# Kernel tuning notes

Measured on AMD Instinct MI355X. Metric: run time of the kernel, lower is better.

Reference implementation:

```python
import jax, jax.numpy as jnp
import numpy as np

DIM = 1024
HEADS = 16
DHEAD = 64
MAXLEN = 512
B = 8
N = 256   # sequence (x) length
M = 256   # memory (h) length; M + N <= MAXLEN
INNER = HEADS * DHEAD


def setup_inputs() -> dict:
    key = jax.random.key(0)
    ks = jax.random.split(key, 8)
    w = lambda k, shape: jax.random.normal(k, shape, jnp.float32) * 0.02
    return {
        "x": jax.random.normal(ks[0], (B, N, DIM), jnp.float32),
        "h": jax.random.normal(ks[1], (B, M, DIM), jnp.float32),
        "Wqkv": w(ks[2], (DIM, 3 * INNER)),
        "Wkr": w(ks[3], (DIM, INNER)),
        "R": jax.random.normal(ks[4], (2 * MAXLEN, DIM), jnp.float32),
        "u": jax.random.normal(ks[5], (DHEAD,), jnp.float32),
        "v": jax.random.normal(ks[6], (DHEAD,), jnp.float32),
        "Wout": w(ks[7], (INNER, DIM)),
        "max_len": MAXLEN,
    }


def reference(x, h, Wqkv, Wkr, R, u, v, Wout, max_len):
    b, n, dim = x.shape
    m = h.shape[1]
    t = m + n
    scale = DHEAD ** -0.5

    cat = jnp.concatenate([h, x], axis=1)                     # [b, t, dim]
    qkv = cat @ Wqkv                                          # [b, t, 3*inner]
    q, k, val = [s.reshape(b, t, HEADS, DHEAD).transpose(0, 2, 1, 3)
                 for s in jnp.split(qkv, 3, axis=-1)]          # [b, h, t, d]

    # shifts[i, j] = (j - i) mod 2L, sliced as in the torch buffer
    ar = jnp.arange(2 * max_len)
    shifts_full = (ar[None, :] - ar[:, None]) % (2 * max_len)
    shifts = shifts_full[:max_len, :max_len][m:m + n, :t]      # [n, t]

    kr = (R @ Wkr)[shifts]                                    # gather: [n, t, inner]
    kr = kr.reshape(n, t, HEADS, DHEAD).transpose(2, 0, 1, 3)  # [h, n, t, d]

    q = q[:, :, m:]                                           # [b, h, n, d]

    term_a = jnp.einsum('bhnd,bhmd->bhnm', q, k)
    term_b = jnp.einsum('bhnd,hnmd->bhnm', q, kr)
    term_c = jnp.einsum('d,bhmd->bhm', u, k)[:, :, None, :]    # broadcast over n
    term_d = jnp.einsum('d,hnmd->hnm', v, kr)[None]            # broadcast over b
    dots = (term_a + term_b + term_c + term_d) * scale         # [b, h, n, t]

    qi = jnp.arange(n)[:, None]
    jm = jnp.arange(m)[None, :]
    js = jnp.arange(n)[None, :]
    mem_mask = jnp.where(qi > jm, -jnp.inf, 0.0)               # [n, m]
    ar_mask = jnp.where(js > qi, -jnp.inf, 0.0)                # [n, n]
    bias = jnp.concatenate([mem_mask, ar_mask], axis=1)[None, None]  # [1,1,n,t]

    attn = jax.nn.softmax(dots + bias, axis=-1)
    out = jnp.einsum('bhnm,bhmd->bhnd', attn, val)             # [b, h, n, d]
    out = out.transpose(0, 2, 1, 3).reshape(b, n, INNER)
    return out @ Wout
```

## Files before the change

kernel.cpp:

```cpp
#include <hip/hip_runtime.h>
#include <hip/hip_bf16.h>
#include <math.h>

typedef unsigned short u16;
typedef short bf16x8 __attribute__((ext_vector_type(8)));
typedef float f32x4 __attribute__((ext_vector_type(4)));

__device__ __forceinline__ u16 f2b(float f) {
    __hip_bfloat16 h = __float2bfloat16(f);
    return *reinterpret_cast<u16*>(&h);
}
__device__ __forceinline__ float b2f(u16 v) {
    __hip_bfloat16 h;
    *reinterpret_cast<u16*>(&h) = v;
    return __bfloat162float(h);
}

__device__ __forceinline__ void gload_lds16(const void* g, void* l) {
    __builtin_amdgcn_global_load_lds(
        (const __attribute__((address_space(1))) void*)g,
        (__attribute__((address_space(3))) void*)l, 16, 0, 0);
}


struct EpiQKV4 {
    u16 *Q, *Kt, *Vt;
    __device__ void operator()(int rowp, int colp, f32x4 vals) const {
        int b = colp >> 9, pos = colp & 511;
        int sec = rowp >> 10, cc = rowp & 1023;
        int head = cc >> 6, d0 = cc & 63;
        if (sec == 0) {
            if (pos < 256) return;
            ushort4 o;
            o.x = f2b(vals[0] * 0.125f); o.y = f2b(vals[1] * 0.125f);
            o.z = f2b(vals[2] * 0.125f); o.w = f2b(vals[3] * 0.125f);
            *(ushort4*)(Q + (long)((head * 8 + b) * 256 + (pos - 256)) * 64 + d0) = o;
        } else if (sec == 1) {
            ushort4 o;
            o.x = f2b(vals[0]); o.y = f2b(vals[1]);
            o.z = f2b(vals[2]); o.w = f2b(vals[3]);
            *(ushort4*)(Kt + (long)((b * 16 + head) * 512 + pos) * 64 + d0) = o;
        } else {
            #pragma unroll
            for (int r = 0; r < 4; ++r)
                Vt[(long)((b * 16 + head) * 64 + d0 + r) * 512 + pos] = f2b(vals[r]);
        }
    }
};

struct EpiStoreBf {
    u16* C; long ldc; long strideZ;
    __device__ void operator()(int z, int row, int col, float val) const {
        C[(long)z * strideZ + (long)row * ldc + col] = f2b(val);
    }
};

struct EpiStoreF32 {
    float* C; long ldc;
    __device__ void operator()(int z, int row, int col, float val) const {
        C[(long)row * ldc + col] = val;
    }
};


template <typename Epi, bool AF32, bool ADDA, bool ROWMAP>
__device__ __forceinline__ void gemm_bt_body(char* smem, int bx, int by, int bz,
                                             const void* __restrict__ Av, int lda, long strideAz,
                                             const u16* __restrict__ B, int ldb, long strideBz,
                                             int K, Epi epi, const float* __restrict__ av) {
    constexpr int LDT = 56;
    u16* As = (u16*)smem;
    u16* Bs = As + 64 * LDT;
    int n0 = bx * 64, m0 = by * 64, z = bz;
    const u16* Bb = B + (long)z * strideBz + (long)n0 * ldb;
    int tid = threadIdx.x;
    int wave = tid >> 6, lane = tid & 63;
    int wm = wave >> 1, wn = wave & 1;
    int lrow = lane & 15, lquad = lane >> 4;
    int srow = tid >> 2, scol = (tid & 3) * 8;
    f32x4 acc[2][2] = {};
    for (int k0 = 0; k0 < K; k0 += 32) {
        if constexpr (AF32) {
            long arow = m0 + srow;
            if constexpr (ROWMAP) arow = (arow < 256) ? 768 + arow : 0;
            const float* src = (const float*)Av + (long)z * strideAz + arow * lda + k0 + scol;
            float4 f0 = *(const float4*)src;
            float4 f1 = *(const float4*)(src + 4);
            bf16x8 vv;
            vv[0] = (short)f2b(f0.x); vv[1] = (short)f2b(f0.y);
            vv[2] = (short)f2b(f0.z); vv[3] = (short)f2b(f0.w);
            vv[4] = (short)f2b(f1.x); vv[5] = (short)f2b(f1.y);
            vv[6] = (short)f2b(f1.z); vv[7] = (short)f2b(f1.w);
            *(bf16x8*)(As + srow * LDT + scol) = vv;
        } else {
            const u16* Ab = (const u16*)Av + (long)z * strideAz + (long)m0 * lda;
            *(bf16x8*)(As + srow * LDT + scol) = *(const bf16x8*)(Ab + (long)srow * lda + k0 + scol);
        }
        *(bf16x8*)(Bs + srow * LDT + scol) = *(const bf16x8*)(Bb + (long)srow * ldb + k0 + scol);
        __syncthreads();
        bf16x8 af[2], bfr[2];
        #pragma unroll
        for (int mt = 0; mt < 2; ++mt) {
            af[mt] = *(const bf16x8*)(As + (wm * 32 + mt * 16 + lrow) * LDT + lquad * 8);
            if constexpr (ADDA) {
                #pragma unroll
                for (int j = 0; j < 8; ++j)
                    af[mt][j] = (short)f2b(b2f((u16)af[mt][j]) + 0.125f * av[k0 + lquad * 8 + j]);
            }
        }
        #pragma unroll
        for (int nt = 0; nt < 2; ++nt)
            bfr[nt] = *(const bf16x8*)(Bs + (wn * 32 + nt * 16 + lrow) * LDT + lquad * 8);
        #pragma unroll
        for (int mt = 0; mt < 2; ++mt)
            #pragma unroll
            for (int nt = 0; nt < 2; ++nt)
                acc[mt][nt] = __builtin_amdgcn_mfma_f32_16x16x32_bf16(af[mt], bfr[nt], acc[mt][nt], 0, 0, 0);
        __syncthreads();
    }
    #pragma unroll
    for (int mt = 0; mt < 2; ++mt)
        #pragma unroll
        for (int nt = 0; nt < 2; ++nt)
            #pragma unroll
            for (int r = 0; r < 4; ++r) {
                int row = m0 + wm * 32 + mt * 16 + lquad * 4 + r;
                int col = n0 + wn * 32 + nt * 16 + lrow;
                epi(z, row, col, acc[mt][nt][r]);
            }
}

__global__ __launch_bounds__(256) void prep_kernel(const float* __restrict__ x,
                                                   const float* __restrict__ h,
                                                   u16* __restrict__ catBF,
                                                   const float* __restrict__ Wqkv, u16* __restrict__ WqkvT,
                                                   const float* __restrict__ Wkr,  u16* __restrict__ WkrT,
                                                   const float* __restrict__ Wout, u16* __restrict__ WoutT,
                                                   u16* __restrict__ vtGuard) {
    __shared__ float tile[32][33];
    int bid = blockIdx.x, tid = threadIdx.x;
    if (bid == 7168) {
        ((unsigned int*)vtGuard)[tid] = 0u;
        return;
    }
    if (bid < 2048) {
        int idx = (bid * 256 + tid) * 8;
        int c = idx & 1023, r = idx >> 10;
        int b = r >> 9, pos = r & 511;
        const float* src = (pos < 256) ? h + ((long)(b * 256 + pos) * 1024 + c)
                                       : x + ((long)(b * 256 + pos - 256) * 1024 + c);
        float4 f0 = *(const float4*)src;
        float4 f1 = *(const float4*)(src + 4);
        bf16x8 vv;
        vv[0] = (short)f2b(f0.x); vv[1] = (short)f2b(f0.y);
        vv[2] = (short)f2b(f0.z); vv[3] = (short)f2b(f0.w);
        vv[4] = (short)f2b(f1.x); vv[5] = (short)f2b(f1.y);
        vv[6] = (short)f2b(f1.z); vv[7] = (short)f2b(f1.w);
        *(bf16x8*)(catBF + idx) = vv;
        return;
    }
    const float* W; u16* WT; int nb, kb;
    if (bid < 5120) {
        int w = bid - 2048;
        W = Wqkv; WT = WqkvT;
        nb = (w % 96) * 32; kb = (w / 96) * 32;
        int tx = tid & 31, ty = tid >> 5;
        #pragma unroll
        for (int i = 0; i < 32; i += 8)
            tile[ty + i][tx] = W[(long)(kb + ty + i) * 3072 + nb + tx];
    } else {
        int w = bid - 5120;
        if (w < 1024) { W = Wkr; WT = WkrT; }
        else          { W = Wout; WT = WoutT; w -= 1024; }
        nb = (w & 31) * 32; kb = (w >> 5) * 32;
        int tx = tid & 31, ty = tid >> 5;
        #pragma unroll
        for (int i = 0; i < 32; i += 8)
            tile[ty + i][tx] = W[(long)(kb + ty + i) * 1024 + nb + tx];
    }
    __syncthreads();
    int row = tid >> 3;
    int c4 = (tid & 7) * 4;
    ushort4 o;
    o.x = f2b(tile[c4 + 0][row]);
    o.y = f2b(tile[c4 + 1][row]);
    o.z = f2b(tile[c4 + 2][row]);
    o.w = f2b(tile[c4 + 3][row]);
    *(ushort4*)(WT + (long)(nb + row) * 1024 + kb + c4) = o;
}

__global__ __launch_bounds__(256, 4) void qkv_rwg_kernel(const u16* __restrict__ A, const u16* __restrict__ B,
                                                         EpiQKV4 eq,
                                                         const float* __restrict__ R, const u16* __restrict__ WkrT,
                                                         u16* __restrict__ RWg) {
    __shared__ alignas(16) char smem[32768];
    int bid0 = blockIdx.x;
    if (bid0 >= 640) {
        int bid2 = bid0 - 640;
        gemm_bt_body<EpiStoreBf, true, false, true>(smem, bid2 & 15, bid2 >> 4, 0,
            (const void*)R, 1024, 0L, WkrT, 1024, 0L, 1024, EpiStoreBf{RWg, 1024, 0}, nullptr);
        return;
    }
    int xcd = bid0 & 7, s = bid0 >> 3;
    int G = xcd * 10 + (s >> 3);
    int w = s & 7;
    int m0, n0;
    if (G < 64) {
        int nchunk = G >> 4, mrow = G & 15;
        m0 = 1024 + mrow * 128;
        n0 = (nchunk * 8 + w) * 128;
    } else {
        int G2 = G - 64;
        int nchunk = G2 >> 3, mrow = G2 & 7;
        m0 = mrow * 128;
        int c = nchunk * 8 + w;
        n0 = (c >> 1) * 512 + 256 + (c & 1) * 128;
    }
    int tid = threadIdx.x, wave = tid >> 6, lane = tid & 63;
    int wm = wave >> 1, wn = wave & 1;
    int lrow = lane & 15, lquad = lane >> 4;
    const u16* Ab = A + (long)m0 * 1024;
    const u16* Bb = B + (long)n0 * 1024;
    f32x4 acc[4][4] = {};

    auto stage = [&](int buf, int k0) {
        u16* Asb = (u16*)smem + buf * 8192;
        u16* Bsb = Asb + 4096;
        #pragma unroll
        for (int i = 0; i < 2; ++i) {
            int rowb = i * 64 + (tid >> 2);
            int col = k0 + (tid & 3) * 8;
            gload_lds16(Ab + (long)rowb * 1024 + col, Asb + i * 2048 + tid * 8);
            gload_lds16(Bb + (long)rowb * 1024 + col, Bsb + i * 2048 + tid * 8);
        }
    };
    auto compute = [&](int buf) {
        u16* Asb = (u16*)smem + buf * 8192;
        u16* Bsb = Asb + 4096;
        bf16x8 af[4], bfr[4];
        #pragma unroll
        for (int mt = 0; mt < 4; ++mt)
            af[mt] = *(const bf16x8*)(Asb + (wm * 64 + mt * 16 + lrow) * 32 + lquad * 8);
        #pragma unroll
        for (int nt = 0; nt < 4; ++nt)
            bfr[nt] = *(const bf16x8*)(Bsb + (wn * 64 + nt * 16 + lrow) * 32 + lquad * 8);
        #pragma unroll
        for (int mt = 0; mt < 4; ++mt)
            #pragma unroll
            for (int nt = 0; nt < 4; ++nt)
                acc[mt][nt] = __builtin_amdgcn_mfma_f32_16x16x32_bf16(af[mt], bfr[nt], acc[mt][nt], 0, 0, 0);
    };

    stage(0, 0);
    stage(1, 32);
    for (int t = 0; t < 31; ++t) {
        asm volatile("s_waitcnt vmcnt(4)" ::: "memory");
        __builtin_amdgcn_sched_barrier(0);
        __builtin_amdgcn_s_barrier();
        __builtin_amdgcn_sched_barrier(0);
        compute(t & 1);
        __builtin_amdgcn_sched_barrier(0);
        __builtin_amdgcn_s_barrier();
        __builtin_amdgcn_sched_barrier(0);
        if (t < 30) stage(t & 1, (t + 2) * 32);
    }
    asm volatile("s_waitcnt vmcnt(0)" ::: "memory");
    __builtin_amdgcn_sched_barrier(0);
    __builtin_amdgcn_s_barrier();
    __builtin_amdgcn_sched_barrier(0);
    compute(1);

    #pragma unroll
    for (int mt = 0; mt < 4; ++mt)
        #pragma unroll
        for (int nt = 0; nt < 4; ++nt) {
            int rowp = m0 + wm * 64 + mt * 16 + lquad * 4;
            int colp = n0 + wn * 64 + nt * 16 + lrow;
            eq(rowp, colp, acc[mt][nt]);
        }
}

__global__ __launch_bounds__(256) void outproj_kernel(const u16* __restrict__ A,
                                                      const u16* __restrict__ B,
                                                      float* __restrict__ out) {
    __shared__ alignas(16) char smem[14336];
    gemm_bt_body<EpiStoreF32, false, false, false>(smem, blockIdx.x, blockIdx.y, 0,
        (const void*)A, 1024, 0L, B, 1024, 0L, 1024, EpiStoreF32{out, 1024}, nullptr);
}

__global__ __launch_bounds__(256, 4) void attn_kernel(const u16* __restrict__ Qs,
                                                      const u16* __restrict__ Kt,
                                                      const u16* __restrict__ VT,
                                                      const u16* __restrict__ RWg,
                                                      const float* __restrict__ uvec,
                                                      const float* __restrict__ vvec,
                                                      u16* __restrict__ attnOut) {
    constexpr int LDSW = 328;
    __shared__ alignas(16) u16 SQ[32 * LDSW];
    __shared__ float red[2][4][32];
    int id = blockIdx.x;
    int bh = id & 127, it = id >> 7;
    int b = bh >> 4, h = bh & 15;
    int i0 = it * 32;
    int w0 = i0;
    int tid = threadIdx.x, wave = tid >> 6, lane = tid & 63;
    int lrow = lane & 15, lquad = lane >> 4;

    bf16x8 aq[2][2], aqv[2][2];
    #pragma unroll
    for (int iu = 0; iu < 2; ++iu) {
        const u16* qbase = Qs + (long)((h * 8 + b) * 256 + i0 + iu * 16 + lrow) * 64;
        bf16x8 q0 = *(const bf16x8*)(qbase + lquad * 8);
        bf16x8 q1 = *(const bf16x8*)(qbase + 32 + lquad * 8);
        #pragma unroll
        for (int j = 0; j < 8; ++j) {
            float f0 = b2f((u16)q0[j]), f1 = b2f((u16)q1[j]);
            aq[iu][0][j]  = (short)f2b(f0 + 0.125f * uvec[lquad * 8 + j]);
            aq[iu][1][j]  = (short)f2b(f1 + 0.125f * uvec[32 + lquad * 8 + j]);
            aqv[iu][0][j] = (short)f2b(f0 + 0.125f * vvec[lquad * 8 + j]);
            aqv[iu][1][j] = (short)f2b(f1 + 0.125f * vvec[32 + lquad * 8 + j]);
        }
    }

    const u16* rwbase = RWg + (long)(wave * 80) * 1024 + h * 64;
    #pragma unroll
    for (int t = 0; t < 5; ++t) {
        const u16* rp = rwbase + (long)(t * 16 + lrow) * 1024;
        bf16x8 br0 = *(const bf16x8*)(rp + lquad * 8);
        bf16x8 br1 = *(const bf16x8*)(rp + 32 + lquad * 8);
        int sc = wave * 80 + t * 16 + lrow;
        #pragma unroll
        for (int iu = 0; iu < 2; ++iu) {
            f32x4 qa = {0.f, 0.f, 0.f, 0.f};
            qa = __builtin_amdgcn_mfma_f32_16x16x32_bf16(aqv[iu][0], br0, qa, 0, 0, 0);
            qa = __builtin_amdgcn_mfma_f32_16x16x32_bf16(aqv[iu][1], br1, qa, 0, 0, 0);
            #pragma unroll
            for (int r = 0; r < 4; ++r)
                SQ[(iu * 16 + lquad * 4 + r) * LDSW + sc] = f2b(qa[r]);
        }
    }

    const u16* kbase = Kt + ((long)bh * 512 + w0 + wave * 80) * 64;
    bf16x8 bk0[5], bk1[5];
    #pragma unroll
    for (int t = 0; t < 5; ++t) {
        const u16* kp = kbase + (long)(t * 16 + lrow) * 64;
        bk0[t] = *(const bf16x8*)(kp + lquad * 8);
        bk1[t] = *(const bf16x8*)(kp + 32 + lquad * 8);
    }
    f32x4 acc[2][5];
    #pragma unroll
    for (int t = 0; t < 5; ++t)
        #pragma unroll
        for (int iu = 0; iu < 2; ++iu) {
            f32x4 a = {0.f, 0.f, 0.f, 0.f};
            a = __builtin_amdgcn_mfma_f32_16x16x32_bf16(aq[iu][0], bk0[t], a, 0, 0, 0);
            a = __builtin_amdgcn_mfma_f32_16x16x32_bf16(aq[iu][1], bk1[t], a, 0, 0, 0);
            acc[iu][t] = a;
        }
    __syncthreads();

    float m4[2][4];
    #pragma unroll
    for (int iu = 0; iu < 2; ++iu)
        #pragma unroll
        for (int r = 0; r < 4; ++r) m4[iu][r] = -1e30f;
    #pragma unroll
    for (int t = 0; t < 5; ++t) {
        int lj = wave * 80 + t * 16 + lrow;
        #pragma unroll
        for (int iu = 0; iu < 2; ++iu)
            #pragma unroll
            for (int r = 0; r < 4; ++r) {
                int rloc = iu * 16 + lquad * 4 + r;
                int d = lj - rloc;
                int dc = d < 0 ? 0 : (d > 256 ? 256 : d);
                bool ok = (unsigned)d <= 256u;
                float val = ok ? acc[iu][t][r] + b2f(SQ[rloc * LDSW + dc]) : -1e30f;
                acc[iu][t][r] = val;
                m4[iu][r] = fmaxf(m4[iu][r], val);
            }
    }
    #pragma unroll
    for (int iu = 0; iu < 2; ++iu)
        #pragma unroll
        for (int r = 0; r < 4; ++r) {
            #pragma unroll
            for (int off = 1; off < 16; off <<= 1)
                m4[iu][r] = fmaxf(m4[iu][r], __shfl_xor(m4[iu][r], off));
            if (lrow == 0) red[0][wave][iu * 16 + lquad * 4 + r] = m4[iu][r];
        }
    __syncthreads();

    float gmax[2][4];
    #pragma unroll
    for (int iu = 0; iu < 2; ++iu)
        #pragma unroll
        for (int r = 0; r < 4; ++r) {
            int row = iu * 16 + lquad * 4 + r;
            gmax[iu][r] = fmaxf(fmaxf(red[0][0][row], red[0][1][row]),
                                fmaxf(red[0][2][row], red[0][3][row]));
        }

    float s4[2][4] = {};
    #pragma unroll
    for (int t = 0; t < 5; ++t) {
        int lj = wave * 80 + t * 16 + lrow;
        #pragma unroll
        for (int iu = 0; iu < 2; ++iu)
            #pragma unroll
            for (int r = 0; r < 4; ++r) {
                float p = __expf(acc[iu][t][r] - gmax[iu][r]);
                s4[iu][r] += p;
                SQ[(iu * 16 + lquad * 4 + r) * LDSW + lj] = f2b(p);
            }
    }
    #pragma unroll
    for (int iu = 0; iu < 2; ++iu)
        #pragma unroll
        for (int r = 0; r < 4; ++r) {
            #pragma unroll
            for (int off = 1; off < 16; off <<= 1)
                s4[iu][r] += __shfl_xor(s4[iu][r], off);
            if (lrow == 0) red[1][wave][iu * 16 + lquad * 4 + r] = s4[iu][r];
        }
    __syncthreads();

    const u16* vbase = VT + ((long)bh * 64 + wave * 16 + lrow) * 512 + w0;
    f32x4 oacc[2] = {};
    bf16x8 vp[10];
    #pragma unroll
    for (int t = 0; t < 10; ++t)
        vp[t] = *(const bf16x8*)(vbase + t * 32 + lquad * 8);
    #pragma unroll
    for (int t = 0; t < 10; ++t)
        #pragma unroll
        for (int iu = 0; iu < 2; ++iu) {
            bf16x8 ap = *(const bf16x8*)(SQ + (iu * 16 + lrow) * LDSW + t * 32 + lquad * 8);
            oacc[iu] = __builtin_amdgcn_mfma_f32_16x16x32_bf16(ap, vp[t], oacc[iu], 0, 0, 0);
        }
    #pragma unroll
    for (int iu = 0; iu < 2; ++iu)
        #pragma unroll
        for (int r = 0; r < 4; ++r) {
            int row = iu * 16 + lquad * 4 + r;
            float inv = 1.0f / (red[1][0][row] + red[1][1][row] + red[1][2][row] + red[1][3][row]);
            attnOut[(long)(b * 256 + i0 + row) * 1024 + h * 64 + wave * 16 + lrow] = f2b(oacc[iu][r] * inv);
        }
}


extern "C" void kernel_launch(void* const* d_in, const int* in_sizes, int n_in,
                              void* d_out, int out_size, void* d_ws, size_t ws_size,
                              hipStream_t stream) {
    (void)in_sizes; (void)n_in; (void)out_size; (void)ws_size;
    const float* x    = (const float*)d_in[0];
    const float* h    = (const float*)d_in[1];
    const float* Wqkv = (const float*)d_in[2];
    const float* Wkr  = (const float*)d_in[3];
    const float* R    = (const float*)d_in[4];
    const float* u    = (const float*)d_in[5];
    const float* v    = (const float*)d_in[6];
    const float* Wout = (const float*)d_in[7];
    float* out = (float*)d_out;

    char* ws = (char*)d_ws;
    size_t off = 0;
    auto alloc = [&](size_t bytes) -> void* {
        void* p = ws + off;
        off = (off + bytes + 255) & ~(size_t)255;
        return p;
    };
    u16* catBF  = (u16*)alloc(4096L * 1024 * 2);
    u16* WqkvT  = (u16*)alloc(3072L * 1024 * 2);
    u16* WkrT   = (u16*)alloc(1024L * 1024 * 2);
    u16* WoutT  = (u16*)alloc(1024L * 1024 * 2);
    u16* RWg    = (u16*)alloc(320L * 1024 * 2);
    u16* Q      = (u16*)alloc(16L * 8 * 256 * 64 * 2);
    u16* Kt     = (u16*)alloc(8L * 16 * 512 * 64 * 2);
    u16* VT     = (u16*)alloc(8L * 16 * 64 * 512 * 2 + 1024);
    u16* attnO  = (u16*)alloc(2048L * 1024 * 2);
    u16* vtGuard = VT + 8L * 16 * 64 * 512;

    prep_kernel<<<7169, 256, 0, stream>>>(x, h, catBF, Wqkv, WqkvT, Wkr, WkrT, Wout, WoutT, vtGuard);
    qkv_rwg_kernel<<<720, 256, 0, stream>>>(WqkvT, catBF, EpiQKV4{Q, Kt, VT}, R, WkrT, RWg);
    attn_kernel<<<1024, 256, 0, stream>>>(Q, Kt, VT, RWg, u, v, attnO);
    outproj_kernel<<<dim3(16, 32), 256, 0, stream>>>(attnO, WoutT, out);
}
```

Before: 166.8 us.

## Halve QKV GEMM tile to 64x128 and pipeline out-projection with LDS DMA

The QKV GEMM tile shrinks from 128x128 to 64x128 with one wave per 32-column strip, doubling the block count to 1280 and raising the occupancy hint to 5. The RWg blocks now come first in the grid instead of last, so they are scheduled early. The out-projection is rewritten from the generic register-staged GEMM body into a double-buffered global_load_lds pipeline like the QKV kernel, and the unused ADDA path is removed. The aim is better CU fill and latency hiding, at the cost of less data reuse per block in the QKV GEMM.

```diff
diff --git a/kernel.cpp b/kernel.cpp
--- a/kernel.cpp
+++ b/kernel.cpp
@@ -55,19 +55,12 @@
     }
 };
 
-struct EpiStoreF32 {
-    float* C; long ldc;
-    __device__ void operator()(int z, int row, int col, float val) const {
-        C[(long)row * ldc + col] = val;
-    }
-};
-
-
-template <typename Epi, bool AF32, bool ADDA, bool ROWMAP>
+
+template <typename Epi, bool AF32, bool ROWMAP>
 __device__ __forceinline__ void gemm_bt_body(char* smem, int bx, int by, int bz,
                                              const void* __restrict__ Av, int lda, long strideAz,
                                              const u16* __restrict__ B, int ldb, long strideBz,
-                                             int K, Epi epi, const float* __restrict__ av) {
+                                             int K, Epi epi) {
     constexpr int LDT = 56;
     u16* As = (u16*)smem;
     u16* Bs = As + 64 * LDT;
@@ -100,14 +93,8 @@
         __syncthreads();
         bf16x8 af[2], bfr[2];
         #pragma unroll
-        for (int mt = 0; mt < 2; ++mt) {
+        for (int mt = 0; mt < 2; ++mt)
             af[mt] = *(const bf16x8*)(As + (wm * 32 + mt * 16 + lrow) * LDT + lquad * 8);
-            if constexpr (ADDA) {
-                #pragma unroll
-                for (int j = 0; j < 8; ++j)
-                    af[mt][j] = (short)f2b(b2f((u16)af[mt][j]) + 0.125f * av[k0 + lquad * 8 + j]);
-            }
-        }
         #pragma unroll
         for (int nt = 0; nt < 2; ++nt)
             bfr[nt] = *(const bf16x8*)(Bs + (wn * 32 + nt * 16 + lrow) * LDT + lquad * 8);
@@ -189,72 +176,135 @@
     *(ushort4*)(WT + (long)(nb + row) * 1024 + kb + c4) = o;
 }
 
-__global__ __launch_bounds__(256, 4) void qkv_rwg_kernel(const u16* __restrict__ A, const u16* __restrict__ B,
+__global__ __launch_bounds__(256, 5) void qkv_rwg_kernel(const u16* __restrict__ A, const u16* __restrict__ B,
                                                          EpiQKV4 eq,
                                                          const float* __restrict__ R, const u16* __restrict__ WkrT,
                                                          u16* __restrict__ RWg) {
-    __shared__ alignas(16) char smem[32768];
+    __shared__ alignas(16) char smem[24576];
     int bid0 = blockIdx.x;
-    if (bid0 >= 640) {
-        int bid2 = bid0 - 640;
-        gemm_bt_body<EpiStoreBf, true, false, true>(smem, bid2 & 15, bid2 >> 4, 0,
-            (const void*)R, 1024, 0L, WkrT, 1024, 0L, 1024, EpiStoreBf{RWg, 1024, 0}, nullptr);
+    if (bid0 < 80) {
+        gemm_bt_body<EpiStoreBf, true, true>(smem, bid0 & 15, bid0 >> 4, 0,
+            (const void*)R, 1024, 0L, WkrT, 1024, 0L, 1024, EpiStoreBf{RWg, 1024, 0});
         return;
     }
-    int xcd = bid0 & 7, s = bid0 >> 3;
-    int G = xcd * 10 + (s >> 3);
-    int w = s & 7;
+    int q = bid0 - 80;
+    int xcd = q & 7, s = q >> 3;
+    int G = xcd * 10 + (s >> 4);
+    int w = s & 15;
     int m0, n0;
     if (G < 64) {
         int nchunk = G >> 4, mrow = G & 15;
-        m0 = 1024 + mrow * 128;
-        n0 = (nchunk * 8 + w) * 128;
+        m0 = 1024 + mrow * 128 + (w & 1) * 64;
+        n0 = (nchunk * 8 + (w >> 1)) * 128;
     } else {
         int G2 = G - 64;
         int nchunk = G2 >> 3, mrow = G2 & 7;
-        m0 = mrow * 128;
-        int c = nchunk * 8 + w;
+        m0 = mrow * 128 + (w & 1) * 64;
+        int c = nchunk * 8 + (w >> 1);
         n0 = (c >> 1) * 512 + 256 + (c & 1) * 128;
     }
+    int tid = threadIdx.x, wave = tid >> 6, lane = tid & 63;
+    int lrow = lane & 15, lquad = lane >> 4;
+    const u16* Ab = A + (long)m0 * 1024;
+    const u16* Bb = B + (long)n0 * 1024;
+    f32x4 acc[4][2] = {};
+
+    auto stage = [&](int buf, int k0) {
+        u16* Asb = (u16*)smem + buf * 6144;
+        u16* Bsb = Asb + 2048;
+        int row = tid >> 2, col = k0 + (tid & 3) * 8;
+        gload_lds16(Ab + (long)row * 1024 + col, Asb + tid * 8);
+        #pragma unroll
+        for (int i = 0; i < 2; ++i)
+            gload_lds16(Bb + (long)(i * 64 + row) * 1024 + col, Bsb + i * 2048 + tid * 8);
+    };
+    auto compute = [&](int buf) {
+        u16* Asb = (u16*)smem + buf * 6144;
+        u16* Bsb = Asb + 2048;
+        bf16x8 af[4], bfr[2];
+        #pragma unroll
+        for (int mt = 0; mt < 4; ++mt)
+            af[mt] = *(const bf16x8*)(Asb + (mt * 16 + lrow) * 32 + lquad * 8);
+        #pragma unroll
+        for (int nt = 0; nt < 2; ++nt)
+            bfr[nt] = *(const bf16x8*)(Bsb + (wave * 32 + nt * 16 + lrow) * 32 + lquad * 8);
+        #pragma unroll
+        for (int mt = 0; mt < 4; ++mt)
+            #pragma unroll
+            for (int nt = 0; nt < 2; ++nt)
+                acc[mt][nt] = __builtin_amdgcn_mfma_f32_16x16x32_bf16(af[mt], bfr[nt], acc[mt][nt], 0, 0, 0);
+    };
+
+    stage(0, 0);
+    stage(1, 32);
+    for (int t = 0; t < 31; ++t) {
+        asm volatile("s_waitcnt vmcnt(3)" ::: "memory");
+        __builtin_amdgcn_sched_barrier(0);
+        __builtin_amdgcn_s_barrier();
+        __builtin_amdgcn_sched_barrier(0);
+        compute(t & 1);
+        __builtin_amdgcn_sched_barrier(0);
+        __builtin_amdgcn_s_barrier();
+        __builtin_amdgcn_sched_barrier(0);
+        if (t < 30) stage(t & 1, (t + 2) * 32);
+    }
+    asm volatile("s_waitcnt vmcnt(0)" ::: "memory");
+    __builtin_amdgcn_sched_barrier(0);
+    __builtin_amdgcn_s_barrier();
+    __builtin_amdgcn_sched_barrier(0);
+    compute(1);
+
+    #pragma unroll
+    for (int mt = 0; mt < 4; ++mt)
+        #pragma unroll
+        for (int nt = 0; nt < 2; ++nt) {
+            int rowp = m0 + mt * 16 + lquad * 4;
+            int colp = n0 + wave * 32 + nt * 16 + lrow;
+            eq(rowp, colp, acc[mt][nt]);
+        }
+}
+
+__global__ __launch_bounds__(256, 4) void outproj_kernel(const u16* __restrict__ A,
+                                                         const u16* __restrict__ B,
+                                                         float* __restrict__ out) {
+    __shared__ alignas(16) char smem[16384];
+    int bid = blockIdx.x;
+    int n0 = (bid & 15) * 64, m0 = (bid >> 4) * 64;
     int tid = threadIdx.x, wave = tid >> 6, lane = tid & 63;
     int wm = wave >> 1, wn = wave & 1;
     int lrow = lane & 15, lquad = lane >> 4;
     const u16* Ab = A + (long)m0 * 1024;
     const u16* Bb = B + (long)n0 * 1024;
-    f32x4 acc[4][4] = {};
+    f32x4 acc[2][2] = {};
 
     auto stage = [&](int buf, int k0) {
-        u16* Asb = (u16*)smem + buf * 8192;
-        u16* Bsb = Asb + 4096;
-        #pragma unroll
-        for (int i = 0; i < 2; ++i) {
-            int rowb = i * 64 + (tid >> 2);
-            int col = k0 + (tid & 3) * 8;
-            gload_lds16(Ab + (long)rowb * 1024 + col, Asb + i * 2048 + tid * 8);
-            gload_lds16(Bb + (long)rowb * 1024 + col, Bsb + i * 2048 + tid * 8);
-        }
+        u16* Asb = (u16*)smem + buf * 4096;
+        u16* Bsb = Asb + 2048;
+        int row = tid >> 2, col = k0 + (tid & 3) * 8;
+        gload_lds16(Ab + (long)row * 1024 + col, Asb + tid * 8);
+        gload_lds16(Bb + (long)row * 1024 + col, Bsb + tid * 8);
     };
     auto compute = [&](int buf) {
-        u16* Asb = (u16*)smem + buf * 8192;
-        u16* Bsb = Asb + 4096;
-        bf16x8 af[4], bfr[4];
-        #pragma unroll
-        for (int mt = 0; mt < 4; ++mt)
-            af[mt] = *(const bf16x8*)(Asb + (wm * 64 + mt * 16 + lrow) * 32 + lquad * 8);
-        #pragma unroll
-        for (int nt = 0; nt < 4; ++nt)
-            bfr[nt] = *(const bf16x8*)(Bsb + (wn * 64 + nt * 16 + lrow) * 32 + lquad * 8);
-        #pragma unroll
-        for (int mt = 0; mt < 4; ++mt)
-            #pragma unroll
-            for (int nt = 0; nt < 4; ++nt)
+        u16* Asb = (u16*)smem + buf * 4096;
+        u16* Bsb = Asb + 2048;
+        bf16x8 af[2], bfr[2];
+        #pragma unroll
+        for (int mt = 0; mt < 2; ++mt)
+            af[mt] = *(const bf16x8*)(Asb + (wm * 32 + mt * 16 + lrow) * 32 + lquad * 8);
+        #pragma unroll
+        for (int nt = 0; nt < 2; ++nt)
+            bfr[nt] = *(const bf16x8*)(Bsb + (wn * 32 + nt * 16 + lrow) * 32 + lquad * 8);
+        #pragma unroll
+        for (int mt = 0; mt < 2; ++mt)
+            #pragma unroll
+            for (int nt = 0; nt < 2; ++nt)
                 acc[mt][nt] = __builtin_amdgcn_mfma_f32_16x16x32_bf16(af[mt], bfr[nt], acc[mt][nt], 0, 0, 0);
     };
 
     stage(0, 0);
     stage(1, 32);
     for (int t = 0; t < 31; ++t) {
-        asm volatile("s_waitcnt vmcnt(4)" ::: "memory");
+        asm volatile("s_waitcnt vmcnt(2)" ::: "memory");
         __builtin_amdgcn_sched_barrier(0);
         __builtin_amdgcn_s_barrier();
         __builtin_amdgcn_sched_barrier(0);
@@ -271,21 +321,13 @@
     compute(1);
 
     #pragma unroll
-    for (int mt = 0; mt < 4; ++mt)
-        #pragma unroll
-        for (int nt = 0; nt < 4; ++nt) {
-            int rowp = m0 + wm * 64 + mt * 16 + lquad * 4;
-            int colp = n0 + wn * 64 + nt * 16 + lrow;
-            eq(rowp, colp, acc[mt][nt]);
-        }
-}
-
-__global__ __launch_bounds__(256) void outproj_kernel(const u16* __restrict__ A,
-                                                      const u16* __restrict__ B,
-                                                      float* __restrict__ out) {
-    __shared__ alignas(16) char smem[14336];
-    gemm_bt_body<EpiStoreF32, false, false, false>(smem, blockIdx.x, blockIdx.y, 0,
-        (const void*)A, 1024, 0L, B, 1024, 0L, 1024, EpiStoreF32{out, 1024}, nullptr);
+    for (int mt = 0; mt < 2; ++mt)
+        #pragma unroll
+        for (int nt = 0; nt < 2; ++nt)
+            #pragma unroll
+            for (int r = 0; r < 4; ++r)
+                out[(long)(m0 + wm * 32 + mt * 16 + lquad * 4 + r) * 1024
+                    + n0 + wn * 32 + nt * 16 + lrow] = acc[mt][nt][r];
 }
 
 __global__ __launch_bounds__(256, 4) void attn_kernel(const u16* __restrict__ Qs,
@@ -483,7 +525,7 @@
     u16* vtGuard = VT + 8L * 16 * 64 * 512;
 
     prep_kernel<<<7169, 256, 0, stream>>>(x, h, catBF, Wqkv, WqkvT, Wkr, WkrT, Wout, WoutT, vtGuard);
-    qkv_rwg_kernel<<<720, 256, 0, stream>>>(WqkvT, catBF, EpiQKV4{Q, Kt, VT}, R, WkrT, RWg);
+    qkv_rwg_kernel<<<1360, 256, 0, stream>>>(WqkvT, catBF, EpiQKV4{Q, Kt, VT}, R, WkrT, RWg);
     attn_kernel<<<1024, 256, 0, stream>>>(Q, Kt, VT, RWg, u, v, attnO);
-    outproj_kernel<<<dim3(16, 32), 256, 0, stream>>>(attnO, WoutT, out);
-}
+    outproj_kernel<<<512, 256, 0, stream>>>(attnO, WoutT, out);
+}
```

Measured after the change: 168.8 us. No clear change (+1.2%).
